# Kernel optimization log

Measured on AMD Instinct MI355X. Metric: run time of the kernel, lower is better.

Reference implementation:

```python
import jax, jax.numpy as jnp
import numpy as np

MAX_VAL = 1000000000000.0


def setup_inputs() -> dict:
    key = jax.random.key(0)
    k1, k2, k3, k4 = jax.random.split(key, 4)
    B, H, N, D = 2, 16, 2048, 64
    query = jax.random.normal(k1, (B, H, N, D), dtype=jnp.float32)
    key_t = jax.random.normal(k2, (B, H, N, D), dtype=jnp.float32)
    value = jax.random.normal(k3, (B, H, N, D), dtype=jnp.float32)
    mask = jax.random.randint(k4, (B, 1, 1, N), 0, 2).astype(bool)
    return {"query": query, "key": key_t, "value": value, "mask": mask,
            "global_num": 8, "window_size": 64}


def reference(query, key, value, mask, global_num, window_size):
    # query/key/value: [B, H, N, D]; mask: [B, 1, 1, N] bool (True = keep)
    B, H, N, D = query.shape
    scale = 1.0 / jnp.sqrt(jnp.asarray(D, dtype=query.dtype))

    # split heads: first global_num are global, rest are local (windowed)
    q_g, k_g, v_g = query[:, :global_num], key[:, :global_num], value[:, :global_num]
    q_l, k_l, v_l = query[:, global_num:], key[:, global_num:], value[:, global_num:]

    # ---- global heads: dense masked attention ----
    scores_g = jnp.einsum('bhqd,bhkd->bhqk', q_g, k_g) * scale
    scores_g = jnp.where(mask, scores_g, -MAX_VAL)
    p_g = jax.nn.softmax(scores_g, axis=-1)
    out_g = jnp.einsum('bhqk,bhkd->bhqd', p_g, v_l[:, :0]) if False else jnp.einsum('bhqk,bhkd->bhqd', p_g, v_g)

    # ---- local heads: window-banded mask on top of padding mask ----
    pos = jnp.arange(N)
    distance = jnp.abs(pos[None, :] - pos[:, None])  # [N, N]
    band = (distance <= window_size)                 # [N, N] bool
    mask_l = mask & band                             # [B, 1, N, N]
    scores_l = jnp.einsum('bhqd,bhkd->bhqk', q_l, k_l) * scale
    scores_l = jnp.where(mask_l, scores_l, -MAX_VAL)
    p_l = jax.nn.softmax(scores_l, axis=-1)
    out_l = jnp.einsum('bhqk,bhkd->bhqd', p_l, v_l)

    out = jnp.concatenate([out_g, out_l], axis=1)  # [B, H, N, D]
    return (out, p_g, p_l)
```

## Files before the change

kernel.cpp:

```cpp
#include <hip/hip_runtime.h>
#include <stdint.h>

typedef __attribute__((ext_vector_type(8))) __bf16 bf16x8;
typedef __attribute__((ext_vector_type(4))) float f32x4;
typedef __attribute__((ext_vector_type(4))) int i32x4;

#define DEVI static __device__ __forceinline__

constexpr int NN = 2048;
constexpr int DD = 64;
constexpr int NH = 16;
constexpr int NG = 8;
constexpr float SCALE = 0.125f;
constexpr float NEGBIG = -1.0e12f;
constexpr size_t OUT_ELEMS = (size_t)2 * NH * NN * DD;
constexpr size_t PG_ELEMS  = (size_t)2 * NG * NN * NN;
constexpr size_t T_ELEMS   = (size_t)2 * NH * NN * DD;
constexpr size_t WS_NEED   = 5 * T_ELEMS * sizeof(__bf16);

struct Frag { bf16x8 hi, lo; };

DEVI Frag make_frag(const float* p) {
  f32x4 a = *(const f32x4*)p;
  f32x4 b = *(const f32x4*)(p + 4);
  Frag f;
#pragma unroll
  for (int j = 0; j < 8; j++) {
    float x = (j < 4) ? a[j] : b[j - 4];
    __bf16 h = (__bf16)x;
    f.hi[j] = h;
    f.lo[j] = (__bf16)(x - (float)h);
  }
  return f;
}

DEVI f32x4 mfma(bf16x8 a, bf16x8 b, f32x4 c) {
  return __builtin_amdgcn_mfma_f32_16x16x32_bf16(a, b, c, 0, 0, 0);
}

struct KT { bf16x8 hi[2][2]; bf16x8 lo[2][2]; i32x4 mv[2]; };
struct VT { bf16x8 v[4]; };

template <bool PRE>
DEVI void load_kt(KT& kt, const __bf16* khi, const __bf16* klo,
                  const float* kp, const int* mp, int wc, int li, int qi) {
#pragma unroll
  for (int Mt = 0; Mt < 2; Mt++)
#pragma unroll
    for (int ks = 0; ks < 2; ks++) {
      const size_t off = (size_t)(wc + Mt * 16 + li) * DD + ks * 32 + qi * 8;
      if constexpr (PRE) {
        kt.hi[Mt][ks] = *(const bf16x8*)(khi + off);
        kt.lo[Mt][ks] = *(const bf16x8*)(klo + off);
      } else {
        Frag f = make_frag(kp + off);
        kt.hi[Mt][ks] = f.hi;
        kt.lo[Mt][ks] = f.lo;
      }
    }
  kt.mv[0] = *(const i32x4*)(mp + wc + qi * 4);
  kt.mv[1] = *(const i32x4*)(mp + wc + 16 + qi * 4);
}

template <bool PRE>
DEVI void load_vt(VT& vt, const __bf16* vtp, const float* vp, int wc, int li, int qi) {
  if constexpr (PRE) {
#pragma unroll
    for (int dt = 0; dt < 4; dt++)
      vt.v[dt] = *(const bf16x8*)(vtp + (size_t)(dt * 16 + li) * NN + wc + qi * 8);
  } else {
#pragma unroll
    for (int dt = 0; dt < 4; dt++)
#pragma unroll
      for (int j = 0; j < 8; j++)
        vt.v[dt][j] = (__bf16)vp[(size_t)(wc + qi * 8 + j) * DD + dt * 16 + li];
  }
}

template <bool LOC>
DEVI void tileA(const KT& kt, const Frag qf[2][2], int wc, int rb, int li, int qi,
                float* m, float* l) {
#pragma unroll
  for (int rs = 0; rs < 2; rs++) {
    f32x4 acc[2];
#pragma unroll
    for (int Mt = 0; Mt < 2; Mt++) {
      f32x4 c = {0.f, 0.f, 0.f, 0.f};
#pragma unroll
      for (int ks = 0; ks < 2; ks++) {
        c = mfma(kt.hi[Mt][ks], qf[rs][ks].hi, c);
        c = mfma(kt.hi[Mt][ks], qf[rs][ks].lo, c);
        c = mfma(kt.lo[Mt][ks], qf[rs][ks].hi, c);
      }
      acc[Mt] = c;
    }
    const int row = rb + rs * 16 + li;
    float vals[8];
#pragma unroll
    for (int Mt = 0; Mt < 2; Mt++)
#pragma unroll
      for (int r = 0; r < 4; r++) {
        const int col = wc + Mt * 16 + qi * 4 + r;
        bool ok = (kt.mv[Mt][r] != 0);
        if constexpr (LOC) { int d = row - col; if (d < 0) d = -d; ok = ok && (d <= 64); }
        vals[Mt * 4 + r] = ok ? acc[Mt][r] * SCALE : NEGBIG;
      }
    float mx = vals[0];
#pragma unroll
    for (int j = 1; j < 8; j++) mx = fmaxf(mx, vals[j]);
    const float mn = fmaxf(m[rs], mx);
    float s = 0.f;
#pragma unroll
    for (int j = 0; j < 8; j++) s += __expf(vals[j] - mn);
    l[rs] = l[rs] * __expf(m[rs] - mn) + s;
    m[rs] = mn;
  }
}

template <bool LOC>
DEVI void tileB(const KT& kt, const VT& vt, const Frag qf[2][2], int wc, int rb,
                int li, int qi, const float* m, const float* rl,
                f32x4 (&o)[2][4], float* pp, int srcA, int srcB, bool selB) {
#pragma unroll
  for (int rs = 0; rs < 2; rs++) {
    f32x4 acc[2];
#pragma unroll
    for (int Mt = 0; Mt < 2; Mt++) {
      f32x4 c = {0.f, 0.f, 0.f, 0.f};
#pragma unroll
      for (int ks = 0; ks < 2; ks++) {
        c = mfma(kt.hi[Mt][ks], qf[rs][ks].hi, c);
        c = mfma(kt.hi[Mt][ks], qf[rs][ks].lo, c);
        c = mfma(kt.lo[Mt][ks], qf[rs][ks].hi, c);
      }
      acc[Mt] = c;
    }
    const int row = rb + rs * 16 + li;
    float pf[8];
#pragma unroll
    for (int Mt = 0; Mt < 2; Mt++)
#pragma unroll
      for (int r = 0; r < 4; r++) {
        const int col = wc + Mt * 16 + qi * 4 + r;
        bool ok = (kt.mv[Mt][r] != 0);
        if constexpr (LOC) { int d = row - col; if (d < 0) d = -d; ok = ok && (d <= 64); }
        const float vv = ok ? acc[Mt][r] * SCALE : NEGBIG;
        pf[Mt * 4 + r] = __expf(vv - m[rs]) * rl[rs];
      }
    float pa[8];
#pragma unroll
    for (int j = 0; j < 8; j++) {
      const int src = (j < 4) ? srcA : srcB;
      const float v0 = __shfl(pf[0 + (j & 3)], src);
      const float v1 = __shfl(pf[4 + (j & 3)], src);
      pa[j] = selB ? v1 : v0;
    }
    float* prow = pp + (size_t)(rb + rs * 16 + li) * NN + wc + qi * 8;
    *(f32x4*)prow       = (f32x4){pa[0], pa[1], pa[2], pa[3]};
    *(f32x4*)(prow + 4) = (f32x4){pa[4], pa[5], pa[6], pa[7]};
    bf16x8 pb;
#pragma unroll
    for (int j = 0; j < 8; j++) pb[j] = (__bf16)pa[j];
#pragma unroll
    for (int dt = 0; dt < 4; dt++)
      o[rs][dt] = mfma(pb, vt.v[dt], o[rs][dt]);
  }
}

__global__ __launch_bounds__(256)
void prep(const float* __restrict__ Q, const float* __restrict__ K,
          const float* __restrict__ V, __bf16* __restrict__ W) {
  const int bid = blockIdx.x;
  if (bid < 4096) {
    const float* src = (bid < 2048) ? Q : K;
    __bf16* hi = W + ((bid < 2048) ? (size_t)0 : 2 * T_ELEMS);
    __bf16* lo = hi + T_ELEMS;
    const size_t base = ((size_t)(bid & 2047) * 256 + threadIdx.x) * 8;
    f32x4 a = *(const f32x4*)(src + base);
    f32x4 b = *(const f32x4*)(src + base + 4);
    bf16x8 h, l;
#pragma unroll
    for (int j = 0; j < 8; j++) {
      float x = (j < 4) ? a[j] : b[j - 4];
      __bf16 hh = (__bf16)x;
      h[j] = hh;
      l[j] = (__bf16)(x - (float)hh);
    }
    *(bf16x8*)(hi + base) = h;
    *(bf16x8*)(lo + base) = l;
  } else {
    __bf16* vt = W + 4 * T_ELEMS;
    const int t  = (bid - 4096) * 256 + (int)threadIdx.x;
    const int ng = t & 63;
    const int dh = t >> 6;
    const int d  = dh & 63;
    const int bh = dh >> 6;
    const float* vp = V + (size_t)bh * NN * DD;
    __bf16* dst = vt + ((size_t)bh * DD + d) * NN + ng * 32;
    bf16x8 o[4];
#pragma unroll
    for (int j = 0; j < 32; j++)
      o[j >> 3][j & 7] = (__bf16)vp[(size_t)(ng * 32 + j) * DD + d];
#pragma unroll
    for (int k = 0; k < 4; k++) *(bf16x8*)(dst + k * 8) = o[k];
  }
}

template <bool PRE>
__global__ __launch_bounds__(256, 2)
void wattn(const float* __restrict__ Q, const float* __restrict__ K,
           const float* __restrict__ V, const int* __restrict__ MSK,
           float* __restrict__ OUT, const __bf16* __restrict__ W) {
  const int bid = blockIdx.x;
  const bool loc = bid >= 256;
  const int lb = loc ? bid - 256 : bid;
  const int bh = lb >> 4;
  const int b  = bh >> 3;
  const int hh = bh & 7;
  const int h  = loc ? (hh + 8) : hh;
  const int wave = (int)(threadIdx.x >> 6);
  const int lane = (int)(threadIdx.x & 63);
  const int qi = lane >> 4;
  const int li = lane & 15;
  const int rb = (lb & 15) * 128 + wave * 32;

  const size_t tb = ((size_t)(b * NH + h) * NN) * DD;
  const float* qp = Q + tb;
  const float* kp = K + tb;
  const float* vp = V + tb;
  const __bf16* qhi = W + tb;
  const __bf16* qlo = W + T_ELEMS + tb;
  const __bf16* khi = W + 2 * T_ELEMS + tb;
  const __bf16* klo = W + 3 * T_ELEMS + tb;
  const __bf16* vtp = W + 4 * T_ELEMS + (size_t)(b * NH + h) * DD * NN;
  const int*   mp = MSK + (size_t)b * NN;
  float* op = OUT + tb;
  float* pp = OUT + OUT_ELEMS + (loc ? PG_ELEMS : (size_t)0)
                  + ((size_t)(b * NG + hh) * NN) * NN;

  Frag qf[2][2];
#pragma unroll
  for (int rs = 0; rs < 2; rs++)
#pragma unroll
    for (int ks = 0; ks < 2; ks++) {
      const size_t off = (size_t)(rb + rs * 16 + li) * DD + ks * 32 + qi * 8;
      if constexpr (PRE) {
        qf[rs][ks].hi = *(const bf16x8*)(qhi + off);
        qf[rs][ks].lo = *(const bf16x8*)(qlo + off);
      } else {
        qf[rs][ks] = make_frag(qp + off);
      }
    }

  float m[2] = {NEGBIG, NEGBIG};
  float l[2] = {0.f, 0.f};

  if (!loc) {
    KT ka, kb;
    load_kt<PRE>(ka, khi, klo, kp, mp, 0, li, qi);
#pragma unroll 1
    for (int t = 0; t < 64; t += 2) {
      load_kt<PRE>(kb, khi, klo, kp, mp, (t + 1) * 32, li, qi);
      tileA<false>(ka, qf, t * 32, rb, li, qi, m, l);
      const int wn = (t + 2 < 64) ? (t + 2) * 32 : 63 * 32;
      load_kt<PRE>(ka, khi, klo, kp, mp, wn, li, qi);
      tileA<false>(kb, qf, (t + 1) * 32, rb, li, qi, m, l);
    }
  } else {
    int wlo = rb - 64; if (wlo < 0) wlo = 0;
    int whi = rb + 96; if (whi > NN) whi = NN;
    const f32x4 z = {0.f, 0.f, 0.f, 0.f};
#pragma unroll 1
    for (int rr = 0; rr < 32; rr++) {
      float* dst = pp + (size_t)(rb + rr) * NN;
#pragma unroll 1
      for (int c = lane * 4; c < NN; c += 256) {
        if (c >= wlo && c < whi) continue;
        *(f32x4*)(dst + c) = z;
      }
    }
    KT ka;
#pragma unroll 1
    for (int t = 0; t < 5; t++) {
      const int wc = rb - 64 + 32 * t;
      if ((unsigned)wc >= (unsigned)NN) continue;
      load_kt<PRE>(ka, khi, klo, kp, mp, wc, li, qi);
      tileA<true>(ka, qf, wc, rb, li, qi, m, l);
    }
  }

  float rl[2];
#pragma unroll
  for (int rs = 0; rs < 2; rs++) {
#pragma unroll
    for (int off = 16; off <= 32; off <<= 1) {
      const float mo  = __shfl_xor(m[rs], off);
      const float lo2 = __shfl_xor(l[rs], off);
      const float mn  = fmaxf(m[rs], mo);
      l[rs] = l[rs] * __expf(m[rs] - mn) + lo2 * __expf(mo - mn);
      m[rs] = mn;
    }
    rl[rs] = 1.0f / l[rs];
  }

  f32x4 o[2][4];
#pragma unroll
  for (int rs = 0; rs < 2; rs++)
#pragma unroll
    for (int dt = 0; dt < 4; dt++) o[rs][dt] = (f32x4){0.f, 0.f, 0.f, 0.f};

  const int srcA = (((qi * 2) + 0) & 3) * 16 + li;
  const int srcB = (((qi * 2) + 1) & 3) * 16 + li;
  const bool selB = (qi >> 1) != 0;

  if (!loc) {
    KT ka, kb;
    VT va, vb;
    load_kt<PRE>(ka, khi, klo, kp, mp, 0, li, qi);
    load_vt<PRE>(va, vtp, vp, 0, li, qi);
#pragma unroll 1
    for (int t = 0; t < 64; t += 2) {
      load_kt<PRE>(kb, khi, klo, kp, mp, (t + 1) * 32, li, qi);
      load_vt<PRE>(vb, vtp, vp, (t + 1) * 32, li, qi);
      tileB<false>(ka, va, qf, t * 32, rb, li, qi, m, rl, o, pp, srcA, srcB, selB);
      const int wn = (t + 2 < 64) ? (t + 2) * 32 : 63 * 32;
      load_kt<PRE>(ka, khi, klo, kp, mp, wn, li, qi);
      load_vt<PRE>(va, vtp, vp, wn, li, qi);
      tileB<false>(kb, vb, qf, (t + 1) * 32, rb, li, qi, m, rl, o, pp, srcA, srcB, selB);
    }
  } else {
    KT ka;
    VT va;
#pragma unroll 1
    for (int t = 0; t < 5; t++) {
      const int wc = rb - 64 + 32 * t;
      if ((unsigned)wc >= (unsigned)NN) continue;
      load_kt<PRE>(ka, khi, klo, kp, mp, wc, li, qi);
      load_vt<PRE>(va, vtp, vp, wc, li, qi);
      tileB<true>(ka, va, qf, wc, rb, li, qi, m, rl, o, pp, srcA, srcB, selB);
    }
  }

#pragma unroll
  for (int rs = 0; rs < 2; rs++)
#pragma unroll
    for (int dt = 0; dt < 4; dt++)
#pragma unroll
      for (int r = 0; r < 4; r++) {
        const int row = rb + rs * 16 + qi * 4 + r;
        op[(size_t)row * DD + dt * 16 + li] = o[rs][dt][r];
      }
}

extern "C" void kernel_launch(void* const* d_in, const int* in_sizes, int n_in,
                              void* d_out, int out_size, void* d_ws, size_t ws_size,
                              hipStream_t stream) {
  (void)in_sizes; (void)n_in; (void)out_size;
  const float* Q = (const float*)d_in[0];
  const float* K = (const float*)d_in[1];
  const float* V = (const float*)d_in[2];
  const int*   M = (const int*)d_in[3];
  float* O = (float*)d_out;
  if (ws_size >= WS_NEED && d_ws != nullptr) {
    __bf16* W = (__bf16*)d_ws;
    prep<<<dim3(4608), dim3(256), 0, stream>>>(Q, K, V, W);
    wattn<true><<<dim3(512), dim3(256), 0, stream>>>(Q, K, V, M, O, W);
  } else {
    wattn<false><<<dim3(512), dim3(256), 0, stream>>>(Q, K, V, M, O, nullptr);
  }
}
```

Baseline: 804.9 us.

## Split key range across waves with LDS softmax merge and XCD-aware block remap

Result: faster. 777.4 us (-3.4%).

```diff
diff --git a/kernel.cpp b/kernel.cpp
--- a/kernel.cpp
+++ b/kernel.cpp
@@ -207,22 +207,27 @@
 }
 
 template <bool PRE>
-__global__ __launch_bounds__(256, 2)
+__global__ __launch_bounds__(256, 3)
 void wattn(const float* __restrict__ Q, const float* __restrict__ K,
            const float* __restrict__ V, const int* __restrict__ MSK,
            float* __restrict__ OUT, const __bf16* __restrict__ W) {
-  const int bid = blockIdx.x;
-  const bool loc = bid >= 256;
-  const int lb = loc ? bid - 256 : bid;
-  const int bh = lb >> 4;
+  __shared__ float2 mlS[4][32];
+  __shared__ float  oS[4][32][64];
+
+  const int bid0 = (int)blockIdx.x;
+  const int xcd = bid0 & 7, jj = bid0 >> 3;
+  const int bid = (jj < 128) ? (xcd * 128 + jj) : (1024 + xcd * 128 + (jj - 128));
+  const bool loc = bid >= 1024;
+  const int lb = loc ? bid - 1024 : bid;
+  const int bh = lb >> 6;
   const int b  = bh >> 3;
   const int hh = bh & 7;
   const int h  = loc ? (hh + 8) : hh;
+  const int rb = (lb & 63) * 32;
   const int wave = (int)(threadIdx.x >> 6);
   const int lane = (int)(threadIdx.x & 63);
   const int qi = lane >> 4;
   const int li = lane & 15;
-  const int rb = (lb & 15) * 128 + wave * 32;
 
   const size_t tb = ((size_t)(b * NH + h) * NN) * DD;
   const float* qp = Q + tb;
@@ -238,6 +243,22 @@
   float* pp = OUT + OUT_ELEMS + (loc ? PG_ELEMS : (size_t)0)
                   + ((size_t)(b * NG + hh) * NN) * NN;
 
+  const int cb  = rb - 64;
+  const int wlo = cb < 0 ? 0 : cb;
+  const int whi = (rb + 96 > NN) ? NN : rb + 96;
+
+  if (loc) {
+    const int c0 = (int)threadIdx.x * 8;
+    const f32x4 z = {0.f, 0.f, 0.f, 0.f};
+#pragma unroll 1
+    for (int rr = 0; rr < 32; rr++) {
+      if (c0 >= wlo && c0 < whi) continue;
+      float* dst = pp + (size_t)(rb + rr) * NN + c0;
+      *(f32x4*)dst       = z;
+      *(f32x4*)(dst + 4) = z;
+    }
+  }
+
   Frag qf[2][2];
 #pragma unroll
   for (int rs = 0; rs < 2; rs++)
@@ -256,40 +277,24 @@
   float l[2] = {0.f, 0.f};
 
   if (!loc) {
-    KT ka, kb;
-    load_kt<PRE>(ka, khi, klo, kp, mp, 0, li, qi);
 #pragma unroll 1
-    for (int t = 0; t < 64; t += 2) {
-      load_kt<PRE>(kb, khi, klo, kp, mp, (t + 1) * 32, li, qi);
-      tileA<false>(ka, qf, t * 32, rb, li, qi, m, l);
-      const int wn = (t + 2 < 64) ? (t + 2) * 32 : 63 * 32;
-      load_kt<PRE>(ka, khi, klo, kp, mp, wn, li, qi);
-      tileA<false>(kb, qf, (t + 1) * 32, rb, li, qi, m, l);
+    for (int tt = 0; tt < 16; tt++) {
+      const int wc = wave * 512 + tt * 32;
+      KT kt;
+      load_kt<PRE>(kt, khi, klo, kp, mp, wc, li, qi);
+      tileA<false>(kt, qf, wc, rb, li, qi, m, l);
     }
   } else {
-    int wlo = rb - 64; if (wlo < 0) wlo = 0;
-    int whi = rb + 96; if (whi > NN) whi = NN;
-    const f32x4 z = {0.f, 0.f, 0.f, 0.f};
 #pragma unroll 1
-    for (int rr = 0; rr < 32; rr++) {
-      float* dst = pp + (size_t)(rb + rr) * NN;
-#pragma unroll 1
-      for (int c = lane * 4; c < NN; c += 256) {
-        if (c >= wlo && c < whi) continue;
-        *(f32x4*)(dst + c) = z;
-      }
-    }
-    KT ka;
-#pragma unroll 1
-    for (int t = 0; t < 5; t++) {
-      const int wc = rb - 64 + 32 * t;
+    for (int t = wave; t < 5; t += 4) {
+      const int wc = cb + 32 * t;
       if ((unsigned)wc >= (unsigned)NN) continue;
-      load_kt<PRE>(ka, khi, klo, kp, mp, wc, li, qi);
-      tileA<true>(ka, qf, wc, rb, li, qi, m, l);
-    }
-  }
-
-  float rl[2];
+      KT kt;
+      load_kt<PRE>(kt, khi, klo, kp, mp, wc, li, qi);
+      tileA<true>(kt, qf, wc, rb, li, qi, m, l);
+    }
+  }
+
 #pragma unroll
   for (int rs = 0; rs < 2; rs++) {
 #pragma unroll
@@ -300,7 +305,23 @@
       l[rs] = l[rs] * __expf(m[rs] - mn) + lo2 * __expf(mo - mn);
       m[rs] = mn;
     }
-    rl[rs] = 1.0f / l[rs];
+    if (qi == 0) mlS[wave][rs * 16 + li] = make_float2(m[rs], l[rs]);
+  }
+  __syncthreads();
+
+  float rl[2];
+#pragma unroll
+  for (int rs = 0; rs < 2; rs++) {
+    float mm = NEGBIG, ll = 0.f;
+#pragma unroll
+    for (int w = 0; w < 4; w++) {
+      const float2 p = mlS[w][rs * 16 + li];
+      const float mn = fmaxf(mm, p.x);
+      ll = ll * __expf(mm - mn) + p.y * __expf(p.x - mn);
+      mm = mn;
+    }
+    m[rs] = mm;
+    rl[rs] = 1.0f / ll;
   }
 
   f32x4 o[2][4];
@@ -314,30 +335,25 @@
   const bool selB = (qi >> 1) != 0;
 
   if (!loc) {
-    KT ka, kb;
-    VT va, vb;
-    load_kt<PRE>(ka, khi, klo, kp, mp, 0, li, qi);
-    load_vt<PRE>(va, vtp, vp, 0, li, qi);
 #pragma unroll 1
-    for (int t = 0; t < 64; t += 2) {
-      load_kt<PRE>(kb, khi, klo, kp, mp, (t + 1) * 32, li, qi);
-      load_vt<PRE>(vb, vtp, vp, (t + 1) * 32, li, qi);
-      tileB<false>(ka, va, qf, t * 32, rb, li, qi, m, rl, o, pp, srcA, srcB, selB);
-      const int wn = (t + 2 < 64) ? (t + 2) * 32 : 63 * 32;
-      load_kt<PRE>(ka, khi, klo, kp, mp, wn, li, qi);
-      load_vt<PRE>(va, vtp, vp, wn, li, qi);
-      tileB<false>(kb, vb, qf, (t + 1) * 32, rb, li, qi, m, rl, o, pp, srcA, srcB, selB);
+    for (int tt = 0; tt < 16; tt++) {
+      const int wc = wave * 512 + tt * 32;
+      KT kt;
+      VT vt;
+      load_kt<PRE>(kt, khi, klo, kp, mp, wc, li, qi);
+      load_vt<PRE>(vt, vtp, vp, wc, li, qi);
+      tileB<false>(kt, vt, qf, wc, rb, li, qi, m, rl, o, pp, srcA, srcB, selB);
     }
   } else {
-    KT ka;
-    VT va;
 #pragma unroll 1
-    for (int t = 0; t < 5; t++) {
-      const int wc = rb - 64 + 32 * t;
+    for (int t = wave; t < 5; t += 4) {
+      const int wc = cb + 32 * t;
       if ((unsigned)wc >= (unsigned)NN) continue;
-      load_kt<PRE>(ka, khi, klo, kp, mp, wc, li, qi);
-      load_vt<PRE>(va, vtp, vp, wc, li, qi);
-      tileB<true>(ka, va, qf, wc, rb, li, qi, m, rl, o, pp, srcA, srcB, selB);
+      KT kt;
+      VT vt;
+      load_kt<PRE>(kt, khi, klo, kp, mp, wc, li, qi);
+      load_vt<PRE>(vt, vtp, vp, wc, li, qi);
+      tileB<true>(kt, vt, qf, wc, rb, li, qi, m, rl, o, pp, srcA, srcB, selB);
     }
   }
 
@@ -346,10 +362,23 @@
 #pragma unroll
     for (int dt = 0; dt < 4; dt++)
 #pragma unroll
-      for (int r = 0; r < 4; r++) {
-        const int row = rb + rs * 16 + qi * 4 + r;
-        op[(size_t)row * DD + dt * 16 + li] = o[rs][dt][r];
-      }
+      for (int r = 0; r < 4; r++)
+        oS[wave][rs * 16 + qi * 4 + r][dt * 16 + li] = o[rs][dt][r];
+  __syncthreads();
+
+  const int tid = (int)threadIdx.x;
+  const int rr = tid >> 3;
+  const int d0 = (tid & 7) * 8;
+  f32x4 s0 = {0.f, 0.f, 0.f, 0.f};
+  f32x4 s1 = {0.f, 0.f, 0.f, 0.f};
+#pragma unroll
+  for (int w = 0; w < 4; w++) {
+    const float* qq = &oS[w][rr][d0];
+    s0 += *(const f32x4*)qq;
+    s1 += *(const f32x4*)(qq + 4);
+  }
+  *(f32x4*)(op + (size_t)(rb + rr) * DD + d0)     = s0;
+  *(f32x4*)(op + (size_t)(rb + rr) * DD + d0 + 4) = s1;
 }
 
 extern "C" void kernel_launch(void* const* d_in, const int* in_sizes, int n_in,
@@ -364,8 +393,8 @@
   if (ws_size >= WS_NEED && d_ws != nullptr) {
     __bf16* W = (__bf16*)d_ws;
     prep<<<dim3(4608), dim3(256), 0, stream>>>(Q, K, V, W);
-    wattn<true><<<dim3(512), dim3(256), 0, stream>>>(Q, K, V, M, O, W);
+    wattn<true><<<dim3(2048), dim3(256), 0, stream>>>(Q, K, V, M, O, W);
   } else {
-    wattn<false><<<dim3(512), dim3(256), 0, stream>>>(Q, K, V, M, O, nullptr);
-  }
-}
+    wattn<false><<<dim3(2048), dim3(256), 0, stream>>>(Q, K, V, M, O, nullptr);
+  }
+}
```
